# Kernel optimization log

Hardware: AMD Instinct MI355X
Metric: run time of the kernel (lower is better)

The kernel has to match this reference:

```python
import jax, jax.numpy as jnp
import numpy as np

DIM = 512
NUM_HEADS = 8
HEAD_DIM = DIM // NUM_HEADS
REL_POS_BINS = 961
B, N = 64, 256


def setup_inputs() -> dict:
    key = jax.random.key(0)
    ks = jax.random.split(key, 7)
    x = jax.random.normal(ks[0], (B, N, DIM), dtype=jnp.float32)
    rel_pos_index = jax.random.randint(ks[1], (N, N), 0, REL_POS_BINS)
    s = 1.0 / np.sqrt(DIM)
    qkv_w = jax.random.normal(ks[2], (3 * DIM, DIM), dtype=jnp.float32) * s
    qkv_b = jax.random.normal(ks[3], (3 * DIM,), dtype=jnp.float32) * 0.02
    proj_w = jax.random.normal(ks[4], (DIM, DIM), dtype=jnp.float32) * s
    proj_b = jax.random.normal(ks[5], (DIM,), dtype=jnp.float32) * 0.02
    rel_pos_bias = jax.random.normal(ks[6], (NUM_HEADS, REL_POS_BINS), dtype=jnp.float32) * 0.02
    return {"x": x, "rel_pos_index": rel_pos_index, "qkv_w": qkv_w,
            "qkv_b": qkv_b, "proj_w": proj_w, "proj_b": proj_b,
            "rel_pos_bias": rel_pos_bias}


def reference(x, rel_pos_index, qkv_w, qkv_b, proj_w, proj_b, rel_pos_bias):
    Bn, Nn, C = x.shape
    H, D = NUM_HEADS, HEAD_DIM
    qkv = x @ qkv_w.T + qkv_b                      # (B,N,3C)
    qkv = qkv.reshape(Bn, Nn, 3, H, D).transpose(2, 0, 3, 1, 4)  # (3,B,H,N,D)
    q, k, v = qkv[0], qkv[1], qkv[2]
    scale = 1.0 / jnp.sqrt(jnp.asarray(D, dtype=x.dtype))
    scores = jnp.einsum('bhnd,bhmd->bhnm', q, k) * scale          # (B,H,N,N)
    bias = rel_pos_bias[:, rel_pos_index]                          # (H,N,N) gather
    scores = scores + bias[None]
    attn = jax.nn.softmax(scores, axis=-1)
    out = jnp.einsum('bhnm,bhmd->bhnd', attn, v)                   # (B,H,N,D)
    out = out.transpose(0, 2, 1, 3).reshape(Bn, Nn, C)
    return out @ proj_w.T + proj_b
```

## Files before the change

kernel.cpp:

```cpp
#include <hip/hip_runtime.h>
#include <stdint.h>

#define DIM 512
#define NHEADS 8
#define HDIM 64
#define NBINS 961
#define BATCH 64
#define SEQ 256
#define NTOK (BATCH*SEQ)
#define BHND (BATCH*NHEADS*SEQ*HDIM)

using bf16x8 = __attribute__((ext_vector_type(8))) short;
using f32x4  = __attribute__((ext_vector_type(4))) float;

__device__ __forceinline__ unsigned short f2bf(float f) {
  unsigned u = __float_as_uint(f);
  u += 0x7FFF + ((u >> 16) & 1);
  return (unsigned short)(u >> 16);
}

__device__ __forceinline__ void async16(const void* g, void* lds) {
  __builtin_amdgcn_global_load_lds(
      (const __attribute__((address_space(1))) unsigned int*)g,
      (__attribute__((address_space(3))) unsigned int*)lds,
      16, 0, 0);
}


__global__ void cast_kernel(const float* __restrict__ in,
                            unsigned short* __restrict__ out, int n4) {
  int i = blockIdx.x * 256 + threadIdx.x;
  if (i >= n4) return;
  float4 f = reinterpret_cast<const float4*>(in)[i];
  ushort4 o;
  o.x = f2bf(f.x); o.y = f2bf(f.y); o.z = f2bf(f.z); o.w = f2bf(f.w);
  reinterpret_cast<ushort4*>(out)[i] = o;
}

__global__ void bias_kernel(const int* __restrict__ idx,
                            const float* __restrict__ rpb,
                            float* __restrict__ bf) {
  int i = blockIdx.x * 256 + threadIdx.x;
  if (i >= NHEADS * SEQ * SEQ) return;
  int h = i >> 16;
  int r = i & 65535;
  bf[i] = rpb[h * NBINS + idx[r]];
}


__device__ __forceinline__ void stage_tile(const unsigned short* __restrict__ A,
                                           const unsigned short* __restrict__ Bw,
                                           char* gsm, int buf, int T,
                                           int m0, int n0, int t, int wv) {
  char* As = gsm + buf * 16384;
  char* Bs = As + 8192;
  const int kk = T * 32;
#pragma unroll
  for (int i = 0; i < 2; ++i) {
    int c = t + i * 256;
    int row = c >> 2, ch = c & 3;
    int sch = ch ^ ((row >> 1) & 3);
    const unsigned short* ga = A + (size_t)(m0 + row) * 512 + kk + sch * 8;
    async16(ga, As + (i * 256 + wv * 64) * 16);
    const unsigned short* gb = Bw + (size_t)(n0 + row) * 512 + kk + sch * 8;
    async16(gb, Bs + (i * 256 + wv * 64) * 16);
  }
}

template<int EPI>
__global__ __launch_bounds__(256) void gemm_bt(
    const unsigned short* __restrict__ A,
    const unsigned short* __restrict__ Bw,
    const float* __restrict__ bias,
    void* __restrict__ outp) {
  __shared__ char gsm[32768];
  const int t = threadIdx.x;
  const int lane = t & 63;
  const int l15 = lane & 15, lg = lane >> 4;
  const int m0 = blockIdx.x * 128, n0 = blockIdx.y * 128;
  const int wv = t >> 6;
  const int wm = wv & 1, wn = wv >> 1;

  f32x4 acc[4][4];
  const f32x4 fz = {0.f, 0.f, 0.f, 0.f};
#pragma unroll
  for (int a = 0; a < 4; ++a)
#pragma unroll
    for (int b = 0; b < 4; ++b) acc[a][b] = fz;

  stage_tile(A, Bw, gsm, 0, 0, m0, n0, t, wv);
  stage_tile(A, Bw, gsm, 1, 1, m0, n0, t, wv);

#pragma unroll 2
  for (int T = 0; T < 16; ++T) {
    if (T < 15) asm volatile("s_waitcnt vmcnt(4)" ::: "memory");
    else        asm volatile("s_waitcnt vmcnt(0)" ::: "memory");
    __builtin_amdgcn_s_barrier();
    __builtin_amdgcn_sched_barrier(0);

    char* As = gsm + (T & 1) * 16384;
    char* Bs = As + 8192;
    bf16x8 af[4], bfr[4];
#pragma unroll
    for (int x = 0; x < 4; ++x) {
      int ra = wm * 64 + x * 16 + l15;
      af[x]  = *(const bf16x8*)(As + ra * 64 + ((lg ^ ((ra >> 1) & 3)) * 16));
      int rb = wn * 64 + x * 16 + l15;
      bfr[x] = *(const bf16x8*)(Bs + rb * 64 + ((lg ^ ((rb >> 1) & 3)) * 16));
    }
    asm volatile("s_waitcnt lgkmcnt(0)" ::: "memory");
    __builtin_amdgcn_sched_barrier(0);
    __builtin_amdgcn_s_barrier();

    if (T < 14) stage_tile(A, Bw, gsm, T & 1, T + 2, m0, n0, t, wv);
    __builtin_amdgcn_sched_barrier(0);

    __builtin_amdgcn_s_setprio(1);
#pragma unroll
    for (int mi = 0; mi < 4; ++mi)
#pragma unroll
      for (int ni = 0; ni < 4; ++ni)
        acc[mi][ni] = __builtin_amdgcn_mfma_f32_16x16x32_bf16(af[mi], bfr[ni], acc[mi][ni], 0, 0, 0);
    __builtin_amdgcn_s_setprio(0);
  }

#pragma unroll
  for (int mi = 0; mi < 4; ++mi)
#pragma unroll
    for (int ni = 0; ni < 4; ++ni)
#pragma unroll
      for (int r = 0; r < 4; ++r) {
        int row = m0 + wm * 64 + mi * 16 + lg * 4 + r;
        int col = n0 + wn * 64 + ni * 16 + l15;
        float v = acc[mi][ni][r] + bias[col];
        if (EPI == 0) {
          int which = col >> 9, hd = col & 511;
          int b = row >> 8, n = row & 255;
          ((unsigned short*)outp)[(size_t)which * BHND +
              (((size_t)(b * NHEADS + (hd >> 6)) * SEQ + n) * HDIM) + (hd & 63)] = f2bf(v);
        } else {
          ((float*)outp)[(size_t)row * 512 + col] = v;
        }
      }
}


__global__ __launch_bounds__(512, 2) void attn_kernel(
    const unsigned short* __restrict__ qb,
    const unsigned short* __restrict__ kb,
    const unsigned short* __restrict__ vb,
    const float* __restrict__ biasf,
    unsigned short* __restrict__ aout) {
  extern __shared__ char smem[];
  char* k_s = smem;
  char* v_s = smem + 32768;
  const int t = threadIdx.x, lane = t & 63, w = t >> 6;
  const int l15 = lane & 15, lg = lane >> 4;
  char* P_s = smem + 65536 + w * 4096;
  const int bh = blockIdx.x;
  const int h = bh & 7;
  const int b = bh >> 3;
  const size_t base = (size_t)bh * (SEQ * HDIM);

#pragma unroll
  for (int i = 0; i < 4; ++i) {
    int c = i * 512 + t;
    int row = c >> 3, sl = c & 7;
    bf16x8 val = *(const bf16x8*)(kb + base + (size_t)c * 8);
    *(bf16x8*)(k_s + row * 128 + ((sl * 16) ^ ((row & 7) << 4))) = val;
  }
#pragma unroll
  for (int i = 0; i < 4; ++i) {
    int c = i * 512 + t;
    int key = c >> 3, d0 = (c & 7) * 8;
    bf16x8 val = *(const bf16x8*)(vb + base + (size_t)c * 8);
#pragma unroll
    for (int j = 0; j < 8; ++j) {
      int d = d0 + j;
      int term = (((d & 7) ^ ((d >> 3) & 7)) << 4);
      *(short*)(v_s + d * 512 + ((key * 2) ^ term)) = val[j];
    }
  }
  bf16x8 qa[2][2];
#pragma unroll
  for (int rf = 0; rf < 2; ++rf)
#pragma unroll
    for (int ks = 0; ks < 2; ++ks)
      qa[rf][ks] = *(const bf16x8*)(qb + base + (size_t)(w * 32 + rf * 16 + l15) * 64 + ks * 32 + lg * 8);
  __syncthreads();

  f32x4 accs[2][16];
  const f32x4 fz = {0.f, 0.f, 0.f, 0.f};
#pragma unroll
  for (int a = 0; a < 2; ++a)
#pragma unroll
    for (int c = 0; c < 16; ++c) accs[a][c] = fz;
  __builtin_amdgcn_s_setprio(1);
#pragma unroll
  for (int cf = 0; cf < 16; ++cf) {
    int key = cf * 16 + l15;
#pragma unroll
    for (int ks = 0; ks < 2; ++ks) {
      bf16x8 kf = *(const bf16x8*)(k_s + key * 128 + ((lg * 16 + ks * 64) ^ ((key & 7) << 4)));
      accs[0][cf] = __builtin_amdgcn_mfma_f32_16x16x32_bf16(qa[0][ks], kf, accs[0][cf], 0, 0, 0);
      accs[1][cf] = __builtin_amdgcn_mfma_f32_16x16x32_bf16(qa[1][ks], kf, accs[1][cf], 0, 0, 0);
    }
  }
  __builtin_amdgcn_s_setprio(0);

  const float* bh_ptr = biasf + h * 65536;
#pragma unroll
  for (int rf = 0; rf < 2; ++rf)
#pragma unroll
    for (int r = 0; r < 4; ++r) {
      int n = w * 32 + rf * 16 + lg * 4 + r;
      const float* bp = bh_ptr + n * 256 + l15;
#pragma unroll
      for (int cf = 0; cf < 16; ++cf)
        accs[rf][cf][r] = accs[rf][cf][r] * 0.125f + bp[cf * 16];
    }

  float pinv[2][4];
#pragma unroll
  for (int rf = 0; rf < 2; ++rf)
#pragma unroll
    for (int r = 0; r < 4; ++r) {
      float m = -1e30f;
#pragma unroll
      for (int cf = 0; cf < 16; ++cf) m = fmaxf(m, accs[rf][cf][r]);
#pragma unroll
      for (int off = 1; off < 16; off <<= 1) m = fmaxf(m, __shfl_xor(m, off, 64));
      float s = 0.f;
#pragma unroll
      for (int cf = 0; cf < 16; ++cf) {
        float p = __expf(accs[rf][cf][r] - m);
        accs[rf][cf][r] = p;
        s += p;
      }
#pragma unroll
      for (int off = 1; off < 16; off <<= 1) s += __shfl_xor(s, off, 64);
      pinv[rf][r] = 1.0f / s;
    }

  f32x4 acco[2][4];
#pragma unroll
  for (int a = 0; a < 2; ++a)
#pragma unroll
    for (int c2 = 0; c2 < 4; ++c2) acco[a][c2] = fz;

  for (int ch = 0; ch < 4; ++ch) {
#pragma unroll
    for (int rf = 0; rf < 2; ++rf)
#pragma unroll
      for (int cl = 0; cl < 4; ++cl)
#pragma unroll
        for (int r = 0; r < 4; ++r) {
          int rowl = rf * 16 + lg * 4 + r;
          int ml = cl * 16 + l15;
          float p = accs[rf][ch * 4 + cl][r] * pinv[rf][r];
          *(short*)(P_s + rowl * 128 + ((ml * 2) ^ ((rowl & 7) << 4))) = (short)f2bf(p);
        }
#pragma unroll
    for (int ks = 0; ks < 2; ++ks) {
      bf16x8 pa[2];
#pragma unroll
      for (int rf = 0; rf < 2; ++rf) {
        int row = rf * 16 + l15;
        pa[rf] = *(const bf16x8*)(P_s + row * 128 + ((lg * 16 + ks * 64) ^ ((row & 7) << 4)));
      }
      int keyb = (ch * 64 + ks * 32 + lg * 8) * 2;
      __builtin_amdgcn_s_setprio(1);
#pragma unroll
      for (int df = 0; df < 4; ++df) {
        int d = df * 16 + l15;
        int term = (((d & 7) ^ ((d >> 3) & 7)) << 4);
        bf16x8 vf = *(const bf16x8*)(v_s + d * 512 + (keyb ^ term));
        acco[0][df] = __builtin_amdgcn_mfma_f32_16x16x32_bf16(pa[0], vf, acco[0][df], 0, 0, 0);
        acco[1][df] = __builtin_amdgcn_mfma_f32_16x16x32_bf16(pa[1], vf, acco[1][df], 0, 0, 0);
      }
      __builtin_amdgcn_s_setprio(0);
    }
  }

#pragma unroll
  for (int rf = 0; rf < 2; ++rf)
#pragma unroll
    for (int df = 0; df < 4; ++df)
#pragma unroll
      for (int r = 0; r < 4; ++r) {
        int n = w * 32 + rf * 16 + lg * 4 + r;
        int d = df * 16 + l15;
        aout[((size_t)(b * SEQ + n)) * DIM + h * HDIM + d] = f2bf(acco[rf][df][r]);
      }
}


extern "C" void kernel_launch(void* const* d_in, const int* in_sizes, int n_in,
                              void* d_out, int out_size, void* d_ws, size_t ws_size,
                              hipStream_t stream) {
  const float* x      = (const float*)d_in[0];
  const int*   rpi    = (const int*)d_in[1];
  const float* qkv_w  = (const float*)d_in[2];
  const float* qkv_b  = (const float*)d_in[3];
  const float* proj_w = (const float*)d_in[4];
  const float* proj_b = (const float*)d_in[5];
  const float* rpb    = (const float*)d_in[6];

  char* ws = (char*)d_ws;
  unsigned short* xb    = (unsigned short*)ws;
  unsigned short* wqkv  = (unsigned short*)(ws + 16777216);
  unsigned short* wproj = (unsigned short*)(ws + 18350080);
  float*          biasf = (float*)         (ws + 18874368);
  unsigned short* qkvb  = (unsigned short*)(ws + 20971520);
  unsigned short* aoutb = (unsigned short*)(ws + 71303168);

  cast_kernel<<<8192, 256, 0, stream>>>(x, xb, 2097152);
  cast_kernel<<<768, 256, 0, stream>>>(qkv_w, wqkv, 196608);
  cast_kernel<<<256, 256, 0, stream>>>(proj_w, wproj, 65536);
  bias_kernel<<<2048, 256, 0, stream>>>(rpi, rpb, biasf);

  dim3 g1(128, 12);
  gemm_bt<0><<<g1, 256, 0, stream>>>(xb, wqkv, qkv_b, (void*)qkvb);

  attn_kernel<<<512, 512, 98304, stream>>>(qkvb, qkvb + BHND, qkvb + 2 * (size_t)BHND,
                                           biasf, aoutb);

  dim3 g2(128, 4);
  gemm_bt<1><<<g2, 256, 0, stream>>>(aoutb, wproj, proj_b, d_out);
}
```

Measured before the change: 102.1 us.

## Enlarge GEMM tiles to 256x256 with K64 stages and 512-thread blocks

Replaces the 128x128, K=32 GEMM with a 256x256 tile per 512-thread block and a 64-wide K stage. Both K halves are split so the second half's LDS reads overlap the first half's MFMAs, with double-buffered async global-to-LDS copies using an 8-chunk XOR swizzle. The larger tile raises arithmetic intensity and cuts the number of K iterations and barriers. In exchange each block uses 128KB of LDS, allowing only one block per CU, and the grids shrink to 384 and 128 blocks. That risks under-filling the CUs, especially for the output projection.

```diff
diff --git a/kernel.cpp b/kernel.cpp
--- a/kernel.cpp
+++ b/kernel.cpp
@@ -48,89 +48,108 @@
 }
 
 
-__device__ __forceinline__ void stage_tile(const unsigned short* __restrict__ A,
-                                           const unsigned short* __restrict__ Bw,
-                                           char* gsm, int buf, int T,
-                                           int m0, int n0, int t, int wv) {
-  char* As = gsm + buf * 16384;
-  char* Bs = As + 8192;
-  const int kk = T * 32;
-#pragma unroll
-  for (int i = 0; i < 2; ++i) {
-    int c = t + i * 256;
-    int row = c >> 2, ch = c & 3;
-    int sch = ch ^ ((row >> 1) & 3);
-    const unsigned short* ga = A + (size_t)(m0 + row) * 512 + kk + sch * 8;
-    async16(ga, As + (i * 256 + wv * 64) * 16);
-    const unsigned short* gb = Bw + (size_t)(n0 + row) * 512 + kk + sch * 8;
-    async16(gb, Bs + (i * 256 + wv * 64) * 16);
+__device__ __forceinline__ void stage256(const unsigned short* __restrict__ X,
+                                         int row0, int T, char* slot,
+                                         int t, int wv) {
+#pragma unroll
+  for (int i = 0; i < 4; ++i) {
+    int q = i * 512 + t;
+    int r = q >> 3, c = q & 7;
+    const unsigned short* src = X + (size_t)(row0 + r) * 512 + T * 64 + ((c ^ (r & 7)) * 8);
+    async16(src, slot + (i * 512 + wv * 64) * 16);
   }
 }
 
 template<int EPI>
-__global__ __launch_bounds__(256) void gemm_bt(
+__global__ __launch_bounds__(512, 2) void gemm256(
     const unsigned short* __restrict__ A,
     const unsigned short* __restrict__ Bw,
     const float* __restrict__ bias,
     void* __restrict__ outp) {
-  __shared__ char gsm[32768];
+  extern __shared__ char gsm[];
   const int t = threadIdx.x;
   const int lane = t & 63;
   const int l15 = lane & 15, lg = lane >> 4;
-  const int m0 = blockIdx.x * 128, n0 = blockIdx.y * 128;
   const int wv = t >> 6;
   const int wm = wv & 1, wn = wv >> 1;
-
-  f32x4 acc[4][4];
+  const int m0 = blockIdx.x * 256, n0 = blockIdx.y * 256;
+
+  f32x4 acc[8][4];
   const f32x4 fz = {0.f, 0.f, 0.f, 0.f};
 #pragma unroll
-  for (int a = 0; a < 4; ++a)
+  for (int a = 0; a < 8; ++a)
 #pragma unroll
     for (int b = 0; b < 4; ++b) acc[a][b] = fz;
 
-  stage_tile(A, Bw, gsm, 0, 0, m0, n0, t, wv);
-  stage_tile(A, Bw, gsm, 1, 1, m0, n0, t, wv);
-
-#pragma unroll 2
-  for (int T = 0; T < 16; ++T) {
-    if (T < 15) asm volatile("s_waitcnt vmcnt(4)" ::: "memory");
-    else        asm volatile("s_waitcnt vmcnt(0)" ::: "memory");
+  stage256(A,  m0, 0, gsm,                 t, wv);
+  stage256(Bw, n0, 0, gsm + 65536,         t, wv);
+  stage256(A,  m0, 1, gsm + 32768,         t, wv);
+  stage256(Bw, n0, 1, gsm + 65536 + 32768, t, wv);
+
+#pragma unroll 1
+  for (int T = 0; T < 8; ++T) {
+    char* Ab = gsm + (T & 1) * 32768;
+    char* Bb = gsm + 65536 + (T & 1) * 32768;
+    if (T < 7) asm volatile("s_waitcnt vmcnt(8)" ::: "memory");
+    else       asm volatile("s_waitcnt vmcnt(0)" ::: "memory");
     __builtin_amdgcn_s_barrier();
     __builtin_amdgcn_sched_barrier(0);
 
-    char* As = gsm + (T & 1) * 16384;
-    char* Bs = As + 8192;
-    bf16x8 af[4], bfr[4];
-#pragma unroll
-    for (int x = 0; x < 4; ++x) {
-      int ra = wm * 64 + x * 16 + l15;
-      af[x]  = *(const bf16x8*)(As + ra * 64 + ((lg ^ ((ra >> 1) & 3)) * 16));
-      int rb = wn * 64 + x * 16 + l15;
-      bfr[x] = *(const bf16x8*)(Bs + rb * 64 + ((lg ^ ((rb >> 1) & 3)) * 16));
-    }
+    bf16x8 a0[8], b0[4];
+#pragma unroll
+    for (int mi = 0; mi < 8; ++mi) {
+      int ra = wm * 128 + mi * 16 + l15;
+      a0[mi] = *(const bf16x8*)(Ab + ra * 128 + ((lg ^ (ra & 7)) * 16));
+    }
+#pragma unroll
+    for (int ni = 0; ni < 4; ++ni) {
+      int rb = wn * 64 + ni * 16 + l15;
+      b0[ni] = *(const bf16x8*)(Bb + rb * 128 + ((lg ^ (rb & 7)) * 16));
+    }
+    __builtin_amdgcn_s_setprio(1);
+#pragma unroll
+    for (int mi = 0; mi < 8; ++mi)
+#pragma unroll
+      for (int ni = 0; ni < 4; ++ni)
+        acc[mi][ni] = __builtin_amdgcn_mfma_f32_16x16x32_bf16(a0[mi], b0[ni], acc[mi][ni], 0, 0, 0);
+    __builtin_amdgcn_s_setprio(0);
+    __builtin_amdgcn_sched_barrier(0);
+
+    bf16x8 a1[8], b1[4];
+#pragma unroll
+    for (int mi = 0; mi < 8; ++mi) {
+      int ra = wm * 128 + mi * 16 + l15;
+      a1[mi] = *(const bf16x8*)(Ab + ra * 128 + (((4 + lg) ^ (ra & 7)) * 16));
+    }
+#pragma unroll
+    for (int ni = 0; ni < 4; ++ni) {
+      int rb = wn * 64 + ni * 16 + l15;
+      b1[ni] = *(const bf16x8*)(Bb + rb * 128 + (((4 + lg) ^ (rb & 7)) * 16));
+    }
+    __builtin_amdgcn_sched_barrier(0);
     asm volatile("s_waitcnt lgkmcnt(0)" ::: "memory");
+    __builtin_amdgcn_s_barrier();
+    if (T < 6) {
+      stage256(A,  m0, T + 2, gsm + (T & 1) * 32768,         t, wv);
+      stage256(Bw, n0, T + 2, gsm + 65536 + (T & 1) * 32768, t, wv);
+    }
     __builtin_amdgcn_sched_barrier(0);
-    __builtin_amdgcn_s_barrier();
-
-    if (T < 14) stage_tile(A, Bw, gsm, T & 1, T + 2, m0, n0, t, wv);
-    __builtin_amdgcn_sched_barrier(0);
-
     __builtin_amdgcn_s_setprio(1);
 #pragma unroll
-    for (int mi = 0; mi < 4; ++mi)
+    for (int mi = 0; mi < 8; ++mi)
 #pragma unroll
       for (int ni = 0; ni < 4; ++ni)
-        acc[mi][ni] = __builtin_amdgcn_mfma_f32_16x16x32_bf16(af[mi], bfr[ni], acc[mi][ni], 0, 0, 0);
+        acc[mi][ni] = __builtin_amdgcn_mfma_f32_16x16x32_bf16(a1[mi], b1[ni], acc[mi][ni], 0, 0, 0);
     __builtin_amdgcn_s_setprio(0);
   }
 
 #pragma unroll
-  for (int mi = 0; mi < 4; ++mi)
+  for (int mi = 0; mi < 8; ++mi)
 #pragma unroll
     for (int ni = 0; ni < 4; ++ni)
 #pragma unroll
       for (int r = 0; r < 4; ++r) {
-        int row = m0 + wm * 64 + mi * 16 + lg * 4 + r;
+        int row = m0 + wm * 128 + mi * 16 + lg * 4 + r;
         int col = n0 + wn * 64 + ni * 16 + l15;
         float v = acc[mi][ni][r] + bias[col];
         if (EPI == 0) {
@@ -319,12 +338,12 @@
   cast_kernel<<<256, 256, 0, stream>>>(proj_w, wproj, 65536);
   bias_kernel<<<2048, 256, 0, stream>>>(rpi, rpb, biasf);
 
-  dim3 g1(128, 12);
-  gemm_bt<0><<<g1, 256, 0, stream>>>(xb, wqkv, qkv_b, (void*)qkvb);
+  dim3 g1(64, 6);
+  gemm256<0><<<g1, 512, 131072, stream>>>(xb, wqkv, qkv_b, (void*)qkvb);
 
   attn_kernel<<<512, 512, 98304, stream>>>(qkvb, qkvb + BHND, qkvb + 2 * (size_t)BHND,
                                            biasf, aoutb);
 
-  dim3 g2(128, 4);
-  gemm_bt<1><<<g2, 256, 0, stream>>>(aoutb, wproj, proj_b, d_out);
-}
+  dim3 g2(64, 2);
+  gemm256<1><<<g2, 512, 131072, stream>>>(aoutb, wproj, proj_b, d_out);
+}
```

After: 108.0 us. +5.8%, slower.
